# Kernel tuning notes

Measured on AMD Instinct MI355X. Metric: run time of the kernel, lower is better.

The kernel has to match this reference:

```python
import jax, jax.numpy as jnp
import numpy as np

BATCH, IN_DIM, H, W = 16, 32, 128, 128
BASE_OUT = 32


def setup_inputs() -> dict:
    key = jax.random.key(0)
    k_x, k_w2, k_b2, k_w1, k_b1 = jax.random.split(key, 5)
    x = jax.random.normal(k_x, (BATCH, IN_DIM, H, W), dtype=jnp.float32)
    # Conv2d(input_dim, 4*base_out, 1): weight (4bo, in_dim) after squeezing 1x1 kernel
    s2 = 1.0 / np.sqrt(IN_DIM)
    W2 = jax.random.uniform(k_w2, (4 * BASE_OUT, IN_DIM), jnp.float32, -s2, s2)
    b2 = jax.random.uniform(k_b2, (4 * BASE_OUT,), jnp.float32, -s2, s2)
    # Conv1d(base_out, 4*base_out, 2): weight (4bo, bo, 2)
    s1 = 1.0 / np.sqrt(BASE_OUT * 2)
    W1 = jax.random.uniform(k_w1, (4 * BASE_OUT, BASE_OUT, 2), jnp.float32, -s1, s1)
    b1 = jax.random.uniform(k_b1, (4 * BASE_OUT,), jnp.float32, -s1, s1)
    return {"x": x, "W2": W2, "b2": b2, "W1": W1, "b1": b1}


def reference(x, W2, b2, W1, b1):
    b, c, h, w = x.shape
    bo = W1.shape[1]  # base_out
    # skew: row i of x is placed at columns [i, i+w) of a (h, 2w-1) canvas
    rows = jnp.arange(h)
    cols = rows[:, None] + jnp.arange(w)[None, :]  # (h, w)
    skewed = jnp.zeros((b, c, h, 2 * w - 1), x.dtype).at[:, :, rows[:, None], cols].set(x)
    # 1x1 conv over channels: input-to-state pre-activations
    i2s = jnp.einsum('oc,bchy->bohy', W2, skewed) + b2[None, :, None, None]
    # original loops only over the first w skewed columns
    xs = jnp.moveaxis(i2s[:, :, :, :w], 3, 0)  # (w, b, 4bo, h)
    W1_prev, W1_cur = W1[:, :, 0], W1[:, :, 1]

    def step(carry, xt):
        pc, ph = carry  # (b, bo, h) each
        # Conv1d(kernel=2) on [0, prev_h]: tap 0 sees ph shifted right by one
        ph_shift = jnp.pad(ph, ((0, 0), (0, 0), (1, 0)))[:, :, :-1]
        s2s = (jnp.einsum('oc,bch->boh', W1_prev, ph_shift)
               + jnp.einsum('oc,bch->boh', W1_cur, ph)
               + b1[None, :, None])
        g = xt + s2s
        o = jax.nn.sigmoid(g[:, 0 * bo:1 * bo])
        f = jax.nn.sigmoid(g[:, 1 * bo:2 * bo])
        i = jax.nn.sigmoid(g[:, 2 * bo:3 * bo])
        gg = jnp.tanh(g[:, 3 * bo:4 * bo])
        nc = f * pc + i * gg
        nh = o * jnp.tanh(nc)
        return (nc, nh), nh

    c0 = jnp.zeros((b, bo, h), x.dtype)
    _, hs = jax.lax.scan(step, (c0, c0), xs)  # hs: (w, b, bo, h)
    return jnp.moveaxis(hs, 0, -1)  # (b, bo, h, w)
```

## Files before the change

kernel.cpp:

```cpp
#include <hip/hip_runtime.h>
#include <stdint.h>

#define BATCH 16
#define CIN   32
#define HH    128
#define WW    128
#define BO    32
#define OCH   128
#define NCH   16
#define DEPTH 64

#define PHP   40
#define GBP   132

#define RINGSZ ((size_t)BATCH * NCH * DEPTH * BO * 8)
#define I2SHSZ ((size_t)BATCH * WW * HH * OCH * 2)

typedef _Float16 f16x8 __attribute__((ext_vector_type(8)));
typedef float    f32x4 __attribute__((ext_vector_type(4)));

__global__ __launch_bounds__(256, 4) void i2s_gemm_h(
    const float* __restrict__ x, const float* __restrict__ W2g,
    const float* __restrict__ b2, const float* __restrict__ b1,
    _Float16* __restrict__ i2sh)
{
    const int tid = threadIdx.x;
    const int bx  = blockIdx.x;
    const int b   = bx >> 7;
    const int row = bx & 127;

    __shared__ __attribute__((aligned(16))) float xs[CIN][WW];
    __shared__ __attribute__((aligned(16))) float w2s[CIN][OCH];
    __shared__ float bs[OCH];

    for (int i = tid; i < CIN * OCH; i += 256) {
        const int c = i >> 7, o = i & 127;
        w2s[c][o] = W2g[o * CIN + c];
    }
    if (tid < OCH) bs[tid] = b2[tid] + b1[tid];
    for (int i = tid; i < CIN * WW; i += 256) {
        const int c = i >> 7, t = i & 127;
        xs[c][t] = (t >= row)
            ? x[((size_t)(b * CIN + c) * HH + row) * WW + (t - row)] : 0.f;
    }
    __syncthreads();

    const int tm = tid >> 4;
    const int tn = tid & 15;
    const int t0 = tm * 8, o0 = tn * 8;

    float bv[8];
    *(float4*)&bv[0] = *(const float4*)&bs[o0];
    *(float4*)&bv[4] = *(const float4*)&bs[o0 + 4];
    float acc[8][8];
#pragma unroll
    for (int i = 0; i < 8; ++i)
#pragma unroll
        for (int jj = 0; jj < 8; ++jj) acc[i][jj] = bv[jj];

    for (int c = 0; c < CIN; ++c) {
        float a[8], wv[8];
        *(float4*)&a[0]  = *(const float4*)&xs[c][t0];
        *(float4*)&a[4]  = *(const float4*)&xs[c][t0 + 4];
        *(float4*)&wv[0] = *(const float4*)&w2s[c][o0];
        *(float4*)&wv[4] = *(const float4*)&w2s[c][o0 + 4];
#pragma unroll
        for (int i = 0; i < 8; ++i)
#pragma unroll
            for (int jj = 0; jj < 8; ++jj)
                acc[i][jj] = fmaf(a[i], wv[jj], acc[i][jj]);
    }

#pragma unroll
    for (int i = 0; i < 8; ++i) {
        f16x8 hv;
#pragma unroll
        for (int jj = 0; jj < 8; ++jj) hv[jj] = (_Float16)acc[i][jj];
        *(f16x8*)&i2sh[((size_t)(b * WW + (t0 + i)) * HH + row) * OCH + o0] = hv;
    }
}

__global__ __launch_bounds__(512) void diag_lstm_scan_v10(
    const float* __restrict__ W1g, float* __restrict__ out,
    int* __restrict__ progress, unsigned long long* __restrict__ hand,
    const _Float16* __restrict__ i2sh)
{
    const int tid = threadIdx.x;
    const int l   = tid & 63;
    const int wv  = tid >> 6;
    const int blk = blockIdx.x;
    const int b = (blk & 7) + ((blk >> 7) << 3);
    const int k = (blk >> 3) & (NCH - 1);

    __shared__ __attribute__((aligned(16))) float    phs[2][9][PHP];
    __shared__ __attribute__((aligned(16))) float    gbuf[8][GBP];
    __shared__ __attribute__((aligned(16))) _Float16 ibuf[2][8][OCH];

    for (int i = tid; i < 2 * 9 * PHP; i += 512) ((float*)phs)[i] = 0.f;

    const int n  = l & 15;
    const int kq = l >> 4;
    const int o  = wv * 16 + n;
    f16x8 bw0, bw1;
    {
        const float4 a0 = *(const float4*)&W1g[(size_t)o * 64 + 8 * kq];
        const float4 a1 = *(const float4*)&W1g[(size_t)o * 64 + 8 * kq + 4];
        const float4 c0 = *(const float4*)&W1g[(size_t)o * 64 + 32 + 8 * kq];
        const float4 c1 = *(const float4*)&W1g[(size_t)o * 64 + 32 + 8 * kq + 4];
        bw0[0] = (_Float16)a0.x; bw0[1] = (_Float16)a0.y;
        bw0[2] = (_Float16)a0.z; bw0[3] = (_Float16)a0.w;
        bw0[4] = (_Float16)a1.x; bw0[5] = (_Float16)a1.y;
        bw0[6] = (_Float16)a1.z; bw0[7] = (_Float16)a1.w;
        bw1[0] = (_Float16)c0.x; bw1[1] = (_Float16)c0.y;
        bw1[2] = (_Float16)c0.z; bw1[3] = (_Float16)c0.w;
        bw1[4] = (_Float16)c1.x; bw1[5] = (_Float16)c1.y;
        bw1[6] = (_Float16)c1.z; bw1[7] = (_Float16)c1.w;
    }

    const int r = (2 * wv + (l >> 5)) & 7;
    const int j = l & 31;
    float pc = 0.f, ob0 = 0.f, ob1 = 0.f, ob2 = 0.f;
    float* outrow = out + ((size_t)(b * BO + j) * HH + (k * 8 + r)) * WW;

    const int kprev = (k > 0) ? k - 1 : 0;
    const unsigned long long* srcbase =
        hand + (size_t)((b * NCH + kprev) * DEPTH) * BO + j;
    unsigned long long* dstbase =
        hand + (size_t)((b * NCH + k) * DEPTH) * BO + j;
    int* myprog   = progress + (b * NCH + k);
    int* consprog = myprog + 1;
    unsigned long long pre = 0ull;

    const size_t islab = (size_t)HH * OCH;
    const _Float16* ibase0 = i2sh + ((size_t)(b * WW) * HH + k * 8) * OCH;
    const int ii = tid & 255;
    uint2 pr0 = make_uint2(0, 0), pr1 = make_uint2(0, 0);

    ((unsigned int*)&ibuf[0][0][0])[tid] = ((const unsigned int*)ibase0)[tid];
    if (wv >= 4) {
        pr0 = ((const uint2*)(ibase0 + 1 * islab))[ii];
        pr1 = ((const uint2*)(ibase0 + 2 * islab))[ii];
    }
    __syncthreads();

    for (int t = 0; t < WW; ++t) {
        const int par = t & 1;

        if (k > 0 && t > 0) {
            unsigned long long q = pre;
            while (__any((unsigned)(q >> 32) != (unsigned)t)) {
                q = __hip_atomic_load(&srcbase[(size_t)((t - 1) & (DEPTH - 1)) * BO],
                                      __ATOMIC_RELAXED, __HIP_MEMORY_SCOPE_AGENT);
            }
            if (l < 32) phs[par][0][l] = __uint_as_float((unsigned)q);
            pre = __hip_atomic_load(&srcbase[(size_t)(t & (DEPTH - 1)) * BO],
                                    __ATOMIC_RELAXED, __HIP_MEMORY_SCOPE_AGENT);
            asm volatile("s_waitcnt lgkmcnt(0)" ::: "memory");
        }

        f16x8 af0 = {}; f16x8 af1 = {};
        if (n < 8) {
            const float4 P0 = *(const float4*)&phs[par][n    ][4 * kq];
            const float4 Q0 = *(const float4*)&phs[par][n + 1][4 * kq];
            const float4 P1 = *(const float4*)&phs[par][n    ][16 + 4 * kq];
            const float4 Q1 = *(const float4*)&phs[par][n + 1][16 + 4 * kq];
            af0[0] = (_Float16)P0.x; af0[1] = (_Float16)Q0.x;
            af0[2] = (_Float16)P0.y; af0[3] = (_Float16)Q0.y;
            af0[4] = (_Float16)P0.z; af0[5] = (_Float16)Q0.z;
            af0[6] = (_Float16)P0.w; af0[7] = (_Float16)Q0.w;
            af1[0] = (_Float16)P1.x; af1[1] = (_Float16)Q1.x;
            af1[2] = (_Float16)P1.y; af1[3] = (_Float16)Q1.y;
            af1[4] = (_Float16)P1.z; af1[5] = (_Float16)Q1.z;
            af1[6] = (_Float16)P1.w; af1[7] = (_Float16)Q1.w;
        }

        f32x4 acc = {0.f, 0.f, 0.f, 0.f};
        acc = __builtin_amdgcn_mfma_f32_16x16x32_f16(af0, bw0, acc, 0, 0, 0);
        acc = __builtin_amdgcn_mfma_f32_16x16x32_f16(af1, bw1, acc, 0, 0, 0);

        if (l < 32) {
#pragma unroll
            for (int e = 0; e < 4; ++e)
                gbuf[4 * kq + e][wv * 16 + n] = acc[e];
        }

        if (wv >= 4) {
            ((uint2*)&ibuf[(t + 1) & 1][0][0])[ii] = pr0;
            pr0 = pr1;
            const int t3 = (t + 3 < WW) ? t + 3 : WW - 1;
            pr1 = ((const uint2*)(ibase0 + (size_t)t3 * islab))[ii];
        }
        __syncthreads();

        if (wv < 4) {
            if (wv == 3 && l >= 32 && k < NCH - 1 && (t & 15) == 0 && t >= 48) {
                while (__hip_atomic_load(consprog, __ATOMIC_RELAXED,
                                         __HIP_MEMORY_SCOPE_AGENT) < t - 47) { }
            }
            const float go = gbuf[r][j]      + (float)ibuf[par][r][j];
            const float gf = gbuf[r][32 + j] + (float)ibuf[par][r][32 + j];
            const float gi = gbuf[r][64 + j] + (float)ibuf[par][r][64 + j];
            const float gg = gbuf[r][96 + j] + (float)ibuf[par][r][96 + j];
            const float so = 1.f / (1.f + __expf(-go));
            const float sf = 1.f / (1.f + __expf(-gf));
            const float si = 1.f / (1.f + __expf(-gi));
            const float tg = 2.f / (1.f + __expf(-2.f * gg)) - 1.f;
            const float nc = sf * pc + si * tg;
            const float th = 2.f / (1.f + __expf(-2.f * nc)) - 1.f;
            const float nh = so * th;
            pc = nc;
            phs[par ^ 1][r + 1][j] = nh;

            const int ph4 = t & 3;
            if (ph4 == 0) ob0 = nh;
            else if (ph4 == 1) ob1 = nh;
            else if (ph4 == 2) ob2 = nh;
            else *(float4*)(outrow + (t - 3)) = make_float4(ob0, ob1, ob2, nh);

            if (wv == 3 && l >= 32 && k < NCH - 1) {
                unsigned long long q = ((unsigned long long)(unsigned)(t + 1) << 32)
                                     | (unsigned long long)__float_as_uint(nh);
                __hip_atomic_store(&dstbase[(size_t)(t & (DEPTH - 1)) * BO], q,
                                   __ATOMIC_RELAXED, __HIP_MEMORY_SCOPE_AGENT);
            }
            if (tid == 0) {
                __hip_atomic_store(myprog, t + 1, __ATOMIC_RELAXED,
                                   __HIP_MEMORY_SCOPE_AGENT);
            }
        }
        __syncthreads();
    }
}

__global__ __launch_bounds__(512, 2) void diag_lstm_scan_v4(
    const float* __restrict__ x, const float* __restrict__ W2g,
    const float* __restrict__ b2, const float* __restrict__ W1g,
    const float* __restrict__ b1, float* __restrict__ out,
    int* __restrict__ progress, unsigned long long* __restrict__ hand)
{
    const int tid = threadIdx.x;
    const int l   = tid & 63;
    const int w   = tid >> 6;
    const int blk = blockIdx.x;
    const int b = (blk & 7) + ((blk >> 7) << 3);
    const int k = (blk >> 3) & (NCH - 1);
    const int row = k * 8 + w;

    __shared__ __attribute__((aligned(16))) float phs[2][9][BO];
    __shared__ __attribute__((aligned(16))) float xbuf[8][CIN];
    __shared__ __attribute__((aligned(16))) float gbuf2[8][OCH];

    for (int i = tid; i < 2 * 9 * BO; i += 512) ((float*)phs)[i] = 0.f;

    const int o0 = 2 * l, o1 = 2 * l + 1;
    float w2a[CIN], w2b[CIN], w1pa[CIN], w1ca[CIN], w1pb[CIN], w1cb[CIN];
#pragma unroll
    for (int c = 0; c < CIN; ++c) {
        w2a[c]  = W2g[o0 * CIN + c];
        w2b[c]  = W2g[o1 * CIN + c];
        w1pa[c] = W1g[(o0 * CIN + c) * 2 + 0];
        w1ca[c] = W1g[(o0 * CIN + c) * 2 + 1];
        w1pb[c] = W1g[(o1 * CIN + c) * 2 + 0];
        w1cb[c] = W1g[(o1 * CIN + c) * 2 + 1];
    }
    const float biasA = b2[o0] + b1[o0];
    const float biasB = b2[o1] + b1[o1];

    const int j = l & 31;
    float pc = 0.f, ob0 = 0.f, ob1 = 0.f, ob2 = 0.f;
    float* outrow = out + ((size_t)(b * BO + j) * HH + row) * WW;

    const int kprev = (k > 0) ? k - 1 : 0;
    const unsigned long long* srcbase =
        hand + (size_t)((b * NCH + kprev) * DEPTH) * BO + j;
    unsigned long long* dstbase =
        hand + (size_t)((b * NCH + k) * DEPTH) * BO + j;
    int* myprog   = progress + (b * NCH + k);
    int* consprog = myprog + 1;

    unsigned long long pre = 0ull;
    __syncthreads();

    for (int t = 0; t < WW; ++t) {
        const int par = t & 1;
        if (l < 32) {
            const int wp = t - row;
            xbuf[w][l] = (wp >= 0)
                ? x[((size_t)(b * CIN + l) * HH + row) * WW + wp] : 0.f;
        }
        if (w == 0 && k > 0) {
            if (t > 0) {
                unsigned long long q = pre;
                while (__any((unsigned)(q >> 32) != (unsigned)t)) {
                    q = __hip_atomic_load(&srcbase[(size_t)((t - 1) & (DEPTH - 1)) * BO],
                                          __ATOMIC_RELAXED, __HIP_MEMORY_SCOPE_AGENT);
                }
                if (l < 32) phs[par][0][l] = __uint_as_float((unsigned)q);
            }
            pre = __hip_atomic_load(&srcbase[(size_t)(t & (DEPTH - 1)) * BO],
                                    __ATOMIC_RELAXED, __HIP_MEMORY_SCOPE_AGENT);
        }
        asm volatile("s_waitcnt lgkmcnt(0)" ::: "memory");

        float ga = biasA, gb = biasB;
        {
            const float4* xb4 = (const float4*)(&xbuf[w][0]);
            const float4* pv4 = (const float4*)(&phs[par][w][0]);
            const float4* qv4 = (const float4*)(&phs[par][w + 1][0]);
#pragma unroll
            for (int cc = 0; cc < CIN / 4; ++cc) {
                const float4 xv = xb4[cc];
                const float4 pv = pv4[cc];
                const float4 qv = qv4[cc];
                const float* xs = (const float*)&xv;
                const float* ps = (const float*)&pv;
                const float* qs = (const float*)&qv;
#pragma unroll
                for (int ci = 0; ci < 4; ++ci) {
                    const int c = 4 * cc + ci;
                    ga = fmaf(w2a[c],  xs[ci], ga);
                    gb = fmaf(w2b[c],  xs[ci], gb);
                    ga = fmaf(w1pa[c], ps[ci], ga);
                    gb = fmaf(w1pb[c], ps[ci], gb);
                    ga = fmaf(w1ca[c], qs[ci], ga);
                    gb = fmaf(w1cb[c], qs[ci], gb);
                }
            }
        }
        *(float2*)&gbuf2[w][o0] = make_float2(ga, gb);
        asm volatile("s_waitcnt lgkmcnt(0)" ::: "memory");

        if (l < 32) {
            if (w == 7 && k < NCH - 1 && (t & 15) == 0 && t >= 48) {
                while (__hip_atomic_load(consprog, __ATOMIC_RELAXED,
                                         __HIP_MEMORY_SCOPE_AGENT) < t - 47) { }
            }
            const float go = gbuf2[w][l];
            const float gf = gbuf2[w][32 + l];
            const float gi = gbuf2[w][64 + l];
            const float gg = gbuf2[w][96 + l];
            const float so = 1.f / (1.f + __expf(-go));
            const float sf = 1.f / (1.f + __expf(-gf));
            const float si = 1.f / (1.f + __expf(-gi));
            const float tg = 2.f / (1.f + __expf(-2.f * gg)) - 1.f;
            const float nc = sf * pc + si * tg;
            const float th = 2.f / (1.f + __expf(-2.f * nc)) - 1.f;
            const float nh = so * th;
            pc = nc;
            phs[par ^ 1][w + 1][l] = nh;

            const int ph4 = t & 3;
            if (ph4 == 0) ob0 = nh;
            else if (ph4 == 1) ob1 = nh;
            else if (ph4 == 2) ob2 = nh;
            else *(float4*)(outrow + (t - 3)) = make_float4(ob0, ob1, ob2, nh);

            if (w == 7 && k < NCH - 1) {
                unsigned long long q = ((unsigned long long)(unsigned)(t + 1) << 32)
                                     | (unsigned long long)__float_as_uint(nh);
                __hip_atomic_store(&dstbase[(size_t)(t & (DEPTH - 1)) * BO], q,
                                   __ATOMIC_RELAXED, __HIP_MEMORY_SCOPE_AGENT);
            }
            if (w == 0 && l == 0) {
                __hip_atomic_store(myprog, t + 1, __ATOMIC_RELAXED,
                                   __HIP_MEMORY_SCOPE_AGENT);
            }
        }
        __syncthreads();
    }
}

extern "C" void kernel_launch(void* const* d_in, const int* in_sizes, int n_in,
                              void* d_out, int out_size, void* d_ws, size_t ws_size,
                              hipStream_t stream) {
    const float* x  = (const float*)d_in[0];
    const float* W2 = (const float*)d_in[1];
    const float* b2 = (const float*)d_in[2];
    const float* W1 = (const float*)d_in[3];
    const float* b1 = (const float*)d_in[4];
    float* out = (float*)d_out;

    int* progress = (int*)d_ws;
    unsigned long long* hand = (unsigned long long*)((char*)d_ws + 4096);
    _Float16* i2sh = (_Float16*)((char*)d_ws + 4096 + RINGSZ);

    const size_t need = 4096 + RINGSZ + I2SHSZ;

    hipMemsetAsync(d_ws, 0, 4096 + RINGSZ, stream);

    if (ws_size >= need) {
        hipLaunchKernelGGL(i2s_gemm_h, dim3(BATCH * HH), dim3(256), 0, stream,
                           x, W2, b2, b1, i2sh);
        hipLaunchKernelGGL(diag_lstm_scan_v10, dim3(BATCH * NCH), dim3(512), 0, stream,
                           W1, out, progress, hand, i2sh);
    } else {
        hipLaunchKernelGGL(diag_lstm_scan_v4, dim3(BATCH * NCH), dim3(512), 0, stream,
                           x, W2, b2, W1, b1, out, progress, hand);
    }
}
```

Baseline: 209.8 us.

## Rewrite diagonal LSTM scan as single-wave blocks handling 16 rows each

Replaces the 512-thread scan kernel with a 64-thread single-wavefront kernel per (batch, 16-row chunk), halving the number of row chunks in the pipelined handoff chain. Each wave computes all 128 gate outputs with 16 MFMAs held in registers, keeps hidden state in fp16 LDS, and prefetches i2s values directly into registers, which removes the block-wide barriers and the gbuf/ibuf LDS round trips. The cost is more serial work per wave with fewer waves in flight and a heavier register load. The fallback path is patched to keep its own 16-chunk indexing.

```diff
diff --git a/kernel.cpp b/kernel.cpp
--- a/kernel.cpp
+++ b/kernel.cpp
@@ -7,17 +7,16 @@
 #define WW    128
 #define BO    32
 #define OCH   128
-#define NCH   16
+#define NCH   8
+#define RPC   16
 #define DEPTH 64
-
-#define PHP   40
-#define GBP   132
 
 #define RINGSZ ((size_t)BATCH * NCH * DEPTH * BO * 8)
 #define I2SHSZ ((size_t)BATCH * WW * HH * OCH * 2)
 
-typedef _Float16 f16x8 __attribute__((ext_vector_type(8)));
-typedef float    f32x4 __attribute__((ext_vector_type(4)));
+typedef _Float16 f16x4v __attribute__((ext_vector_type(4)));
+typedef _Float16 f16x8v __attribute__((ext_vector_type(8)));
+typedef float    f32x4v __attribute__((ext_vector_type(4)));
 
 __global__ __launch_bounds__(256, 4) void i2s_gemm_h(
     const float* __restrict__ x, const float* __restrict__ W2g,
@@ -73,162 +72,170 @@
 
 #pragma unroll
     for (int i = 0; i < 8; ++i) {
-        f16x8 hv;
+        f16x8v hv;
 #pragma unroll
         for (int jj = 0; jj < 8; ++jj) hv[jj] = (_Float16)acc[i][jj];
-        *(f16x8*)&i2sh[((size_t)(b * WW + (t0 + i)) * HH + row) * OCH + o0] = hv;
+        *(f16x8v*)&i2sh[((size_t)(b * WW + (t0 + i)) * HH + row) * OCH + o0] = hv;
     }
 }
 
-__global__ __launch_bounds__(512) void diag_lstm_scan_v10(
+__global__ __launch_bounds__(64, 1) void diag_lstm_scan_v11(
     const float* __restrict__ W1g, float* __restrict__ out,
     int* __restrict__ progress, unsigned long long* __restrict__ hand,
     const _Float16* __restrict__ i2sh)
 {
-    const int tid = threadIdx.x;
-    const int l   = tid & 63;
-    const int wv  = tid >> 6;
+    const int l   = threadIdx.x;
     const int blk = blockIdx.x;
-    const int b = (blk & 7) + ((blk >> 7) << 3);
-    const int k = (blk >> 3) & (NCH - 1);
-
-    __shared__ __attribute__((aligned(16))) float    phs[2][9][PHP];
-    __shared__ __attribute__((aligned(16))) float    gbuf[8][GBP];
-    __shared__ __attribute__((aligned(16))) _Float16 ibuf[2][8][OCH];
-
-    for (int i = tid; i < 2 * 9 * PHP; i += 512) ((float*)phs)[i] = 0.f;
-
-    const int n  = l & 15;
-    const int kq = l >> 4;
-    const int o  = wv * 16 + n;
-    f16x8 bw0, bw1;
+    const int b   = blk & 15;
+    const int k   = blk >> 4;
+    const int q   = l >> 4;
+    const int col = l & 15;
+
+    __shared__ _Float16 phs[2][17][40];
+    for (int i = l; i < 2 * 17 * 40; i += 64) (&phs[0][0][0])[i] = (_Float16)0.f;
+
+    f16x8v bw[8][2];
+#pragma unroll
+    for (int nt = 0; nt < 8; ++nt) {
+        const int o = nt * 16 + col;
+#pragma unroll
+        for (int h = 0; h < 2; ++h) {
+            const float4 w0 = *(const float4*)&W1g[(size_t)o * 64 + 32 * h + 8 * q];
+            const float4 w1 = *(const float4*)&W1g[(size_t)o * 64 + 32 * h + 8 * q + 4];
+            f16x8v v;
+            v[0] = (_Float16)w0.x; v[1] = (_Float16)w0.y;
+            v[2] = (_Float16)w0.z; v[3] = (_Float16)w0.w;
+            v[4] = (_Float16)w1.x; v[5] = (_Float16)w1.y;
+            v[6] = (_Float16)w1.z; v[7] = (_Float16)w1.w;
+            bw[nt][h] = v;
+        }
+    }
+
+    const ushort* i2su = (const ushort*)i2sh;
+    ushort u[8][4];
     {
-        const float4 a0 = *(const float4*)&W1g[(size_t)o * 64 + 8 * kq];
-        const float4 a1 = *(const float4*)&W1g[(size_t)o * 64 + 8 * kq + 4];
-        const float4 c0 = *(const float4*)&W1g[(size_t)o * 64 + 32 + 8 * kq];
-        const float4 c1 = *(const float4*)&W1g[(size_t)o * 64 + 32 + 8 * kq + 4];
-        bw0[0] = (_Float16)a0.x; bw0[1] = (_Float16)a0.y;
-        bw0[2] = (_Float16)a0.z; bw0[3] = (_Float16)a0.w;
-        bw0[4] = (_Float16)a1.x; bw0[5] = (_Float16)a1.y;
-        bw0[6] = (_Float16)a1.z; bw0[7] = (_Float16)a1.w;
-        bw1[0] = (_Float16)c0.x; bw1[1] = (_Float16)c0.y;
-        bw1[2] = (_Float16)c0.z; bw1[3] = (_Float16)c0.w;
-        bw1[4] = (_Float16)c1.x; bw1[5] = (_Float16)c1.y;
-        bw1[6] = (_Float16)c1.z; bw1[7] = (_Float16)c1.w;
-    }
-
-    const int r = (2 * wv + (l >> 5)) & 7;
-    const int j = l & 31;
-    float pc = 0.f, ob0 = 0.f, ob1 = 0.f, ob2 = 0.f;
-    float* outrow = out + ((size_t)(b * BO + j) * HH + (k * 8 + r)) * WW;
+        const size_t base = ((size_t)(b * WW + 0) * HH + k * 16 + 4 * q) * OCH + col;
+#pragma unroll
+        for (int nt = 0; nt < 8; ++nt)
+#pragma unroll
+            for (int e = 0; e < 4; ++e)
+                u[nt][e] = i2su[base + (size_t)e * OCH + nt * 16];
+    }
+
+    float pc[2][4], ob0[2][4], ob1[2][4], ob2[2][4];
+#pragma unroll
+    for (int v = 0; v < 2; ++v)
+#pragma unroll
+        for (int e = 0; e < 4; ++e) { pc[v][e] = 0.f; ob0[v][e] = 0.f; ob1[v][e] = 0.f; ob2[v][e] = 0.f; }
 
     const int kprev = (k > 0) ? k - 1 : 0;
-    const unsigned long long* srcbase =
-        hand + (size_t)((b * NCH + kprev) * DEPTH) * BO + j;
-    unsigned long long* dstbase =
-        hand + (size_t)((b * NCH + k) * DEPTH) * BO + j;
+    const unsigned long long* srcring =
+        hand + ((size_t)(b * NCH + kprev) * DEPTH) * BO + l;
+    unsigned long long* dstring =
+        hand + ((size_t)(b * NCH + k) * DEPTH) * BO + col;
     int* myprog   = progress + (b * NCH + k);
     int* consprog = myprog + 1;
     unsigned long long pre = 0ull;
 
-    const size_t islab = (size_t)HH * OCH;
-    const _Float16* ibase0 = i2sh + ((size_t)(b * WW) * HH + k * 8) * OCH;
-    const int ii = tid & 255;
-    uint2 pr0 = make_uint2(0, 0), pr1 = make_uint2(0, 0);
-
-    ((unsigned int*)&ibuf[0][0][0])[tid] = ((const unsigned int*)ibase0)[tid];
-    if (wv >= 4) {
-        pr0 = ((const uint2*)(ibase0 + 1 * islab))[ii];
-        pr1 = ((const uint2*)(ibase0 + 2 * islab))[ii];
-    }
-    __syncthreads();
-
     for (int t = 0; t < WW; ++t) {
-        const int par = t & 1;
+        _Float16 (*PS)[40] = phs[t & 1];
+        _Float16 (*PD)[40] = phs[(t & 1) ^ 1];
 
         if (k > 0 && t > 0) {
-            unsigned long long q = pre;
-            while (__any((unsigned)(q >> 32) != (unsigned)t)) {
-                q = __hip_atomic_load(&srcbase[(size_t)((t - 1) & (DEPTH - 1)) * BO],
-                                      __ATOMIC_RELAXED, __HIP_MEMORY_SCOPE_AGENT);
-            }
-            if (l < 32) phs[par][0][l] = __uint_as_float((unsigned)q);
-            pre = __hip_atomic_load(&srcbase[(size_t)(t & (DEPTH - 1)) * BO],
-                                    __ATOMIC_RELAXED, __HIP_MEMORY_SCOPE_AGENT);
-            asm volatile("s_waitcnt lgkmcnt(0)" ::: "memory");
-        }
-
-        f16x8 af0 = {}; f16x8 af1 = {};
-        if (n < 8) {
-            const float4 P0 = *(const float4*)&phs[par][n    ][4 * kq];
-            const float4 Q0 = *(const float4*)&phs[par][n + 1][4 * kq];
-            const float4 P1 = *(const float4*)&phs[par][n    ][16 + 4 * kq];
-            const float4 Q1 = *(const float4*)&phs[par][n + 1][16 + 4 * kq];
-            af0[0] = (_Float16)P0.x; af0[1] = (_Float16)Q0.x;
-            af0[2] = (_Float16)P0.y; af0[3] = (_Float16)Q0.y;
-            af0[4] = (_Float16)P0.z; af0[5] = (_Float16)Q0.z;
-            af0[6] = (_Float16)P0.w; af0[7] = (_Float16)Q0.w;
-            af1[0] = (_Float16)P1.x; af1[1] = (_Float16)Q1.x;
-            af1[2] = (_Float16)P1.y; af1[3] = (_Float16)Q1.y;
-            af1[4] = (_Float16)P1.z; af1[5] = (_Float16)Q1.z;
-            af1[6] = (_Float16)P1.w; af1[7] = (_Float16)Q1.w;
-        }
-
-        f32x4 acc = {0.f, 0.f, 0.f, 0.f};
-        acc = __builtin_amdgcn_mfma_f32_16x16x32_f16(af0, bw0, acc, 0, 0, 0);
-        acc = __builtin_amdgcn_mfma_f32_16x16x32_f16(af1, bw1, acc, 0, 0, 0);
-
-        if (l < 32) {
-#pragma unroll
-            for (int e = 0; e < 4; ++e)
-                gbuf[4 * kq + e][wv * 16 + n] = acc[e];
-        }
-
-        if (wv >= 4) {
-            ((uint2*)&ibuf[(t + 1) & 1][0][0])[ii] = pr0;
-            pr0 = pr1;
-            const int t3 = (t + 3 < WW) ? t + 3 : WW - 1;
-            pr1 = ((const uint2*)(ibase0 + (size_t)t3 * islab))[ii];
-        }
-        __syncthreads();
-
-        if (wv < 4) {
-            if (wv == 3 && l >= 32 && k < NCH - 1 && (t & 15) == 0 && t >= 48) {
-                while (__hip_atomic_load(consprog, __ATOMIC_RELAXED,
-                                         __HIP_MEMORY_SCOPE_AGENT) < t - 47) { }
-            }
-            const float go = gbuf[r][j]      + (float)ibuf[par][r][j];
-            const float gf = gbuf[r][32 + j] + (float)ibuf[par][r][32 + j];
-            const float gi = gbuf[r][64 + j] + (float)ibuf[par][r][64 + j];
-            const float gg = gbuf[r][96 + j] + (float)ibuf[par][r][96 + j];
-            const float so = 1.f / (1.f + __expf(-go));
-            const float sf = 1.f / (1.f + __expf(-gf));
-            const float si = 1.f / (1.f + __expf(-gi));
-            const float tg = 2.f / (1.f + __expf(-2.f * gg)) - 1.f;
-            const float nc = sf * pc + si * tg;
-            const float th = 2.f / (1.f + __expf(-2.f * nc)) - 1.f;
-            const float nh = so * th;
-            pc = nc;
-            phs[par ^ 1][r + 1][j] = nh;
-
-            const int ph4 = t & 3;
-            if (ph4 == 0) ob0 = nh;
-            else if (ph4 == 1) ob1 = nh;
-            else if (ph4 == 2) ob2 = nh;
-            else *(float4*)(outrow + (t - 3)) = make_float4(ob0, ob1, ob2, nh);
-
-            if (wv == 3 && l >= 32 && k < NCH - 1) {
-                unsigned long long q = ((unsigned long long)(unsigned)(t + 1) << 32)
-                                     | (unsigned long long)__float_as_uint(nh);
-                __hip_atomic_store(&dstbase[(size_t)(t & (DEPTH - 1)) * BO], q,
-                                   __ATOMIC_RELAXED, __HIP_MEMORY_SCOPE_AGENT);
-            }
-            if (tid == 0) {
-                __hip_atomic_store(myprog, t + 1, __ATOMIC_RELAXED,
-                                   __HIP_MEMORY_SCOPE_AGENT);
-            }
-        }
-        __syncthreads();
+            unsigned long long qv = pre;
+            while (__any(l < 32 && (unsigned)(qv >> 32) != (unsigned)t)) {
+                if (l < 32)
+                    qv = __hip_atomic_load(&srcring[(size_t)((t - 1) & 63) * BO],
+                                           __ATOMIC_RELAXED, __HIP_MEMORY_SCOPE_AGENT);
+            }
+            if (l < 32) {
+                PS[0][l] = (_Float16)__uint_as_float((unsigned)qv);
+                pre = __hip_atomic_load(&srcring[(size_t)(t & 63) * BO],
+                                        __ATOMIC_RELAXED, __HIP_MEMORY_SCOPE_AGENT);
+            }
+        }
+
+        const f16x4v r0 = *(const f16x4v*)&PS[col][4 * q];
+        const f16x4v r1 = *(const f16x4v*)&PS[col + 1][4 * q];
+        const f16x4v r2 = *(const f16x4v*)&PS[col][16 + 4 * q];
+        const f16x4v r3 = *(const f16x4v*)&PS[col + 1][16 + 4 * q];
+        f16x8v af0, af1;
+        af0[0] = r0[0]; af0[1] = r1[0]; af0[2] = r0[1]; af0[3] = r1[1];
+        af0[4] = r0[2]; af0[5] = r1[2]; af0[6] = r0[3]; af0[7] = r1[3];
+        af1[0] = r2[0]; af1[1] = r3[0]; af1[2] = r2[1]; af1[3] = r3[1];
+        af1[4] = r2[2]; af1[5] = r3[2]; af1[6] = r2[3]; af1[7] = r3[3];
+
+        f32x4v acc[8];
+#pragma unroll
+        for (int nt = 0; nt < 8; ++nt) {
+#pragma unroll
+            for (int e = 0; e < 4; ++e) {
+                ushort uv = u[nt][e];
+                acc[nt][e] = (float)(*reinterpret_cast<const _Float16*>(&uv));
+            }
+        }
+        {
+            const int tn = (t + 1 < WW) ? t + 1 : WW - 1;
+            const size_t base = ((size_t)(b * WW + tn) * HH + k * 16 + 4 * q) * OCH + col;
+#pragma unroll
+            for (int nt = 0; nt < 8; ++nt)
+#pragma unroll
+                for (int e = 0; e < 4; ++e)
+                    u[nt][e] = i2su[base + (size_t)e * OCH + nt * 16];
+        }
+
+#pragma unroll
+        for (int nt = 0; nt < 8; ++nt) {
+            acc[nt] = __builtin_amdgcn_mfma_f32_16x16x32_f16(af0, bw[nt][0], acc[nt], 0, 0, 0);
+            acc[nt] = __builtin_amdgcn_mfma_f32_16x16x32_f16(af1, bw[nt][1], acc[nt], 0, 0, 0);
+        }
+
+        if (k < NCH - 1 && (t & 15) == 0 && t >= 48 && l == 0) {
+            while (__hip_atomic_load(consprog, __ATOMIC_RELAXED,
+                                     __HIP_MEMORY_SCOPE_AGENT) < t - 47) { }
+        }
+
+#pragma unroll
+        for (int v = 0; v < 2; ++v) {
+#pragma unroll
+            for (int e = 0; e < 4; ++e) {
+                const float go = acc[v][e];
+                const float gf = acc[v + 2][e];
+                const float gi = acc[v + 4][e];
+                const float gg = acc[v + 6][e];
+                const float so = 1.f / (1.f + __expf(-go));
+                const float sf = 1.f / (1.f + __expf(-gf));
+                const float si = 1.f / (1.f + __expf(-gi));
+                const float tg = 2.f / (1.f + __expf(-2.f * gg)) - 1.f;
+                const float nc = sf * pc[v][e] + si * tg;
+                const float th = 2.f / (1.f + __expf(-2.f * nc)) - 1.f;
+                const float nh = so * th;
+                pc[v][e] = nc;
+                PD[4 * q + e + 1][col + 16 * v] = (_Float16)nh;
+
+                const int ph4 = t & 3;
+                if (ph4 == 0)      ob0[v][e] = nh;
+                else if (ph4 == 1) ob1[v][e] = nh;
+                else if (ph4 == 2) ob2[v][e] = nh;
+                else {
+                    *(float4*)(out + ((size_t)(b * BO + col + 16 * v) * HH
+                                      + k * RPC + 4 * q + e) * WW + (t - 3))
+                        = make_float4(ob0[v][e], ob1[v][e], ob2[v][e], nh);
+                }
+
+                if (q == 3 && e == 3 && k < NCH - 1) {
+                    unsigned long long qq =
+                        ((unsigned long long)(unsigned)(t + 1) << 32)
+                      | (unsigned long long)__float_as_uint(nh);
+                    __hip_atomic_store(&dstring[(size_t)(t & 63) * BO + 16 * v], qq,
+                                       __ATOMIC_RELAXED, __HIP_MEMORY_SCOPE_AGENT);
+                }
+            }
+        }
+        if (l == 0) {
+            __hip_atomic_store(myprog, t + 1, __ATOMIC_RELAXED,
+                               __HIP_MEMORY_SCOPE_AGENT);
+        }
     }
 }
 
@@ -243,7 +250,7 @@
     const int w   = tid >> 6;
     const int blk = blockIdx.x;
     const int b = (blk & 7) + ((blk >> 7) << 3);
-    const int k = (blk >> 3) & (NCH - 1);
+    const int k = (blk >> 3) & 15;
     const int row = k * 8 + w;
 
     __shared__ __attribute__((aligned(16))) float phs[2][9][BO];
@@ -272,10 +279,10 @@
 
     const int kprev = (k > 0) ? k - 1 : 0;
     const unsigned long long* srcbase =
-        hand + (size_t)((b * NCH + kprev) * DEPTH) * BO + j;
+        hand + (size_t)((b * 16 + kprev) * DEPTH) * BO + j;
     unsigned long long* dstbase =
-        hand + (size_t)((b * NCH + k) * DEPTH) * BO + j;
-    int* myprog   = progress + (b * NCH + k);
+        hand + (size_t)((b * 16 + k) * DEPTH) * BO + j;
+    int* myprog   = progress + (b * 16 + k);
     int* consprog = myprog + 1;
 
     unsigned long long pre = 0ull;
@@ -331,7 +338,7 @@
         asm volatile("s_waitcnt lgkmcnt(0)" ::: "memory");
 
         if (l < 32) {
-            if (w == 7 && k < NCH - 1 && (t & 15) == 0 && t >= 48) {
+            if (w == 7 && k < 15 && (t & 15) == 0 && t >= 48) {
                 while (__hip_atomic_load(consprog, __ATOMIC_RELAXED,
                                          __HIP_MEMORY_SCOPE_AGENT) < t - 47) { }
             }
@@ -355,7 +362,7 @@
             else if (ph4 == 2) ob2 = nh;
             else *(float4*)(outrow + (t - 3)) = make_float4(ob0, ob1, ob2, nh);
 
-            if (w == 7 && k < NCH - 1) {
+            if (w == 7 && k < 15) {
                 unsigned long long q = ((unsigned long long)(unsigned)(t + 1) << 32)
                                      | (unsigned long long)__float_as_uint(nh);
                 __hip_atomic_store(&dstbase[(size_t)(t & (DEPTH - 1)) * BO], q,
@@ -391,10 +398,11 @@
     if (ws_size >= need) {
         hipLaunchKernelGGL(i2s_gemm_h, dim3(BATCH * HH), dim3(256), 0, stream,
                            x, W2, b2, b1, i2sh);
-        hipLaunchKernelGGL(diag_lstm_scan_v10, dim3(BATCH * NCH), dim3(512), 0, stream,
+        hipLaunchKernelGGL(diag_lstm_scan_v11, dim3(BATCH * NCH), dim3(64), 0, stream,
                            W1, out, progress, hand, i2sh);
     } else {
-        hipLaunchKernelGGL(diag_lstm_scan_v4, dim3(BATCH * NCH), dim3(512), 0, stream,
+        hipMemsetAsync(d_ws, 0, 4096 + (size_t)BATCH * 16 * DEPTH * BO * 8, stream);
+        hipLaunchKernelGGL(diag_lstm_scan_v4, dim3(BATCH * 16), dim3(512), 0, stream,
                            x, W2, b2, W1, b1, out, progress, hand);
     }
 }
```

New measurement: 420.0 us. +100.2%, slower.
